# Kernel optimization log

Measured on AMD Instinct MI355X. Metric: run time of the kernel, lower is better.

The kernel has to match this reference:

```python
import jax, jax.numpy as jnp
import numpy as np

# DeepSpeed FixedSparsityConfig defaults (attention='unidirectional')
BLOCK = 16
NUM_LOCAL_BLOCKS = 4   # local window = 4 blocks = 64 tokens
D_MODEL = 1024
N_HEADS = 16
HEAD_DIM = D_MODEL // N_HEADS


def _block_layout(seq_len: int) -> np.ndarray:
    """Token-level boolean mask [S,S] from the fixed unidirectional block layout.
    Allowed iff: (same 4-block local window AND block_k <= block_q) OR
                 (block_k % 4 == 3 AND block_k <= block_q)  (causal global column).
    Same layout for every head (different_layout_per_head=False)."""
    nb = seq_len // BLOCK
    r = np.arange(nb)
    causal = r[None, :] <= r[:, None]
    same_win = (r[:, None] // NUM_LOCAL_BLOCKS) == (r[None, :] // NUM_LOCAL_BLOCKS)
    glob = (r[None, :] % NUM_LOCAL_BLOCKS) == (NUM_LOCAL_BLOCKS - 1)
    layout = (same_win & causal) | (glob & causal)
    return np.kron(layout, np.ones((BLOCK, BLOCK), dtype=bool))


def setup_inputs() -> dict:
    key = jax.random.key(0)
    ks = jax.random.split(key, 7)
    B, S = 2, 2048
    init = 1.0 / np.sqrt(D_MODEL)
    x = jax.random.normal(ks[0], (B, S, D_MODEL), jnp.float32)
    key_padding_mask = jnp.zeros((B, S), jnp.float32)  # additive mask ('add' mode)
    Wq = jax.random.normal(ks[1], (D_MODEL, D_MODEL), jnp.float32) * init
    Wk = jax.random.normal(ks[2], (D_MODEL, D_MODEL), jnp.float32) * init
    Wv = jax.random.normal(ks[3], (D_MODEL, D_MODEL), jnp.float32) * init
    bq = jax.random.normal(ks[4], (D_MODEL,), jnp.float32) * 0.01
    bk = jax.random.normal(ks[5], (D_MODEL,), jnp.float32) * 0.01
    bv = jax.random.normal(ks[6], (D_MODEL,), jnp.float32) * 0.01
    return dict(x=x, key_padding_mask=key_padding_mask,
                Wq=Wq, bq=bq, Wk=Wk, bk=bk, Wv=Wv, bv=bv)


def reference(x, key_padding_mask, Wq, bq, Wk, bk, Wv, bv):
    B, S, D = x.shape
    q = (x @ Wq + bq).reshape(B, S, N_HEADS, HEAD_DIM)
    k = (x @ Wk + bk).reshape(B, S, N_HEADS, HEAD_DIM)
    v = (x @ Wv + bv).reshape(B, S, N_HEADS, HEAD_DIM)
    scale = HEAD_DIM ** -0.5  # DeepSpeed scales by head_size**-0.5 inside softmax
    scores = jnp.einsum('bqhd,bkhd->bhqk', q, k) * scale
    scores = scores + key_padding_mask[:, None, None, :]
    mask = jnp.asarray(_block_layout(S))  # [S,S] bool; absent blocks excluded from softmax
    scores = jnp.where(mask[None, None], scores, -jnp.inf)
    attn = jax.nn.softmax(scores, axis=-1)
    out = jnp.einsum('bhqk,bkhd->bqhd', attn, v)
    return out.reshape(B, S, D)
```

## Files before the change

kernel.cpp:

```cpp
#include <hip/hip_runtime.h>
#include <hip/hip_bf16.h>

typedef __bf16 bf16;
typedef __bf16 bf16x4 __attribute__((ext_vector_type(4)));
typedef __bf16 bf16x8 __attribute__((ext_vector_type(8)));
typedef float  f32x4  __attribute__((ext_vector_type(4)));

#define D_MODEL 1024
#define S_LEN   2048
#define BATCH   2
#define NH      16
#define HD      64
#define NX ((size_t)BATCH * S_LEN * D_MODEL)

__device__ inline void gl_lds16(const bf16* g, bf16* l) {
    __builtin_amdgcn_global_load_lds(
        (const __attribute__((address_space(1))) void*)g,
        (__attribute__((address_space(3))) void*)l, 16, 0, 0);
}

__global__ __launch_bounds__(256) void cvt_x(
    const float* __restrict__ x, bf16* __restrict__ xb)
{
    const size_t base = ((size_t)blockIdx.x * 256 + threadIdx.x) * 8;
    const float4 a = *(const float4*)(x + base);
    const float4 b = *(const float4*)(x + base + 4);
    bf16x8 o;
    o[0] = (bf16)a.x; o[1] = (bf16)a.y; o[2] = (bf16)a.z; o[3] = (bf16)a.w;
    o[4] = (bf16)b.x; o[5] = (bf16)b.y; o[6] = (bf16)b.z; o[7] = (bf16)b.w;
    *(bf16x8*)(xb + base) = o;
}

__global__ __launch_bounds__(256) void wt_cvt(
    const float* __restrict__ Wq, const float* __restrict__ Wk,
    const float* __restrict__ Wv, bf16* __restrict__ Wt)
{
    const int z = blockIdx.z;
    const float* W = (z == 0) ? Wq : (z == 1) ? Wk : Wv;
    const int k0 = blockIdx.y * 64, n0 = blockIdx.x * 64;

    __shared__ bf16 tile[64 * 72];

    const int r16 = threadIdx.x >> 4, c4 = (threadIdx.x & 15) << 2;

#pragma unroll
    for (int rr = 0; rr < 4; ++rr) {
        const int row = rr * 16 + r16;
        const float4 v = *(const float4*)(W + (size_t)(k0 + row) * D_MODEL + n0 + c4);
        bf16x4 o; o[0] = (bf16)v.x; o[1] = (bf16)v.y; o[2] = (bf16)v.z; o[3] = (bf16)v.w;
        *(bf16x4*)(tile + row * 72 + c4) = o;
    }
    __syncthreads();
#pragma unroll
    for (int rr = 0; rr < 4; ++rr) {
        const int row = rr * 16 + r16;
        bf16x4 o;
#pragma unroll
        for (int j = 0; j < 4; ++j) o[j] = tile[(c4 + j) * 72 + row];
        *(bf16x4*)(Wt + (size_t)(z * D_MODEL + n0 + row) * D_MODEL + k0 + c4) = o;
    }
}

__global__ __launch_bounds__(256) void gemm_bt(
    const bf16* __restrict__ Xb, const bf16* __restrict__ Wt,
    const float* __restrict__ bq, const float* __restrict__ bk,
    const float* __restrict__ bv, bf16* __restrict__ QKV)
{
    const int n0 = blockIdx.x * 128, m0 = blockIdx.y * 128;
    const int z  = n0 >> 10;
    const float* bias = (z == 0) ? bq : (z == 1) ? bk : bv;
    const float scale = (z == 0) ? 0.125f : 1.0f;
    bf16* C = QKV + (size_t)z * NX;
    const int ncol0 = n0 & 1023;

    __shared__ bf16 As[128 * 32];
    __shared__ bf16 Bs[128 * 32];

    const int t = threadIdx.x, wave = t >> 6, lane = t & 63;
    const int wm = wave >> 1, wn = wave & 1;
    const int col = lane & 15, quad = lane >> 4;
    const int srow = t >> 2, sc8 = (t & 3) << 3;

    f32x4 acc[4][4] = {};

    for (int k0 = 0; k0 < D_MODEL; k0 += 32) {
        gl_lds16(Xb + (size_t)(m0 + srow) * D_MODEL + k0 + sc8,      As + wave * 512);
        gl_lds16(Xb + (size_t)(m0 + 64 + srow) * D_MODEL + k0 + sc8, As + 2048 + wave * 512);
        gl_lds16(Wt + (size_t)(n0 + srow) * D_MODEL + k0 + sc8,      Bs + wave * 512);
        gl_lds16(Wt + (size_t)(n0 + 64 + srow) * D_MODEL + k0 + sc8, Bs + 2048 + wave * 512);
        __syncthreads();

        bf16x8 a[4], b[4];
#pragma unroll
        for (int mt = 0; mt < 4; ++mt)
            a[mt] = *(const bf16x8*)(As + (wm * 64 + mt * 16 + col) * 32 + quad * 8);
#pragma unroll
        for (int nt = 0; nt < 4; ++nt)
            b[nt] = *(const bf16x8*)(Bs + (wn * 64 + nt * 16 + col) * 32 + quad * 8);
#pragma unroll
        for (int mt = 0; mt < 4; ++mt)
#pragma unroll
            for (int nt = 0; nt < 4; ++nt)
                acc[mt][nt] = __builtin_amdgcn_mfma_f32_16x16x32_bf16(a[mt], b[nt], acc[mt][nt], 0, 0, 0);
        __syncthreads();
    }

#pragma unroll
    for (int nt = 0; nt < 4; ++nt) {
        const int cgw = ncol0 + wn * 64 + nt * 16 + col;
        const float bsv = bias[cgw];
#pragma unroll
        for (int mt = 0; mt < 4; ++mt)
#pragma unroll
            for (int i = 0; i < 4; ++i) {
                const int rg = m0 + wm * 64 + mt * 16 + quad * 4 + i;
                C[(size_t)rg * D_MODEL + cgw] = (bf16)((acc[mt][nt][i] + bsv) * scale);
            }
    }
}

__global__ __launch_bounds__(256) void sparse_attn64(
    const bf16* __restrict__ Q, const bf16* __restrict__ Kv,
    const bf16* __restrict__ Vv, const float* __restrict__ kpm,
    float* __restrict__ out)
{
    const int w = (gridDim.x - 1) - blockIdx.x;
    const int h = blockIdx.y, b = blockIdx.z;
    const int t = threadIdx.x, wavei = t >> 6, lane = t & 63;
    const int col = lane & 15, quad = lane >> 4;
    const int qb = 4 * w + wavei;

    __shared__ bf16 KbS[2][64 * 72];
    __shared__ bf16 VtS[2][64 * 72];
    __shared__ bf16 Ps[4][16 * 72];

    const size_t qrow = ((size_t)(b * S_LEN + qb * 16 + col)) * D_MODEL + h * HD;
    const bf16x8 aq0 = *(const bf16x8*)(Q + qrow + quad * 8);
    const bf16x8 aq1 = *(const bf16x8*)(Q + qrow + 32 + quad * 8);

    f32x4 o[4] = {};
    float lacc[4] = {0.f, 0.f, 0.f, 0.f};

    const int nGlob = (w + 3) >> 2;
    const int niter = nGlob + 1;

    const int srow = t >> 2, sd16 = (t & 3) << 4;
    const int sg = srow >> 4, sr = srow & 15;
    const int p2 = t & 31, dg8 = (t >> 5) << 3;
    const int key0 = 2 * p2, vg = key0 >> 4, vr = key0 & 15;

    auto kb_of = [&](int it, int g) -> int {
        if (it == nGlob) return 4 * w + g;
        const int j = 4 * it + g;
        return (j < w) ? (4 * j + 3) : 3;
    };

    bf16x8 rk0, rk1, rv0, rv1;
    {
        const size_t krow = ((size_t)(b * S_LEN + kb_of(0, sg) * 16 + sr)) * D_MODEL + h * HD + sd16;
        rk0 = *(const bf16x8*)(Kv + krow);
        rk1 = *(const bf16x8*)(Kv + krow + 8);
        const size_t vrow = ((size_t)(b * S_LEN + kb_of(0, vg) * 16 + vr)) * D_MODEL + h * HD + dg8;
        rv0 = *(const bf16x8*)(Vv + vrow);
        rv1 = *(const bf16x8*)(Vv + vrow + D_MODEL);
        *(bf16x8*)(KbS[0] + srow * 72 + sd16)     = rk0;
        *(bf16x8*)(KbS[0] + srow * 72 + sd16 + 8) = rk1;
#pragma unroll
        for (int j = 0; j < 8; ++j) {
            bf16 pr[2] = { rv0[j], rv1[j] };
            *(unsigned int*)(VtS[0] + (dg8 + j) * 72 + key0) = *(unsigned int*)pr;
        }
    }

    for (int it = 0; it < niter; ++it) {
        __syncthreads();
        const int cur = it & 1, nxt = cur ^ 1;
        const bool more = (it + 1 < niter);
        if (more) {
            const size_t krow = ((size_t)(b * S_LEN + kb_of(it + 1, sg) * 16 + sr)) * D_MODEL + h * HD + sd16;
            rk0 = *(const bf16x8*)(Kv + krow);
            rk1 = *(const bf16x8*)(Kv + krow + 8);
            const size_t vrow = ((size_t)(b * S_LEN + kb_of(it + 1, vg) * 16 + vr)) * D_MODEL + h * HD + dg8;
            rv0 = *(const bf16x8*)(Vv + vrow);
            rv1 = *(const bf16x8*)(Vv + vrow + D_MODEL);
        }

        const bf16* Kb = KbS[cur];
        const bf16* Vt = VtS[cur];

        f32x4 s[4];
        float mval[4];
        bool  val[4];
#pragma unroll
        for (int g = 0; g < 4; ++g) {
            int kb;
            if (it == nGlob) { kb = 4 * w + g; val[g] = (g <= wavei); }
            else { const int j = 4 * it + g; val[g] = (j < w); kb = val[g] ? (4 * j + 3) : 3; }
            mval[g] = kpm[b * S_LEN + kb * 16 + col];
            f32x4 z = {};
            const bf16x8 bk0 = *(const bf16x8*)(Kb + (g * 16 + col) * 72 + quad * 8);
            const bf16x8 bk1 = *(const bf16x8*)(Kb + (g * 16 + col) * 72 + 32 + quad * 8);
            z = __builtin_amdgcn_mfma_f32_16x16x32_bf16(aq0, bk0, z, 0, 0, 0);
            s[g] = __builtin_amdgcn_mfma_f32_16x16x32_bf16(aq1, bk1, z, 0, 0, 0);
        }

#pragma unroll
        for (int i = 0; i < 4; ++i) {
#pragma unroll
            for (int g = 0; g < 4; ++g) {
                const float si = val[g] ? (s[g][i] + mval[g]) : -1e30f;
                const float pv = __expf(si);
                lacc[i] += pv;
                Ps[wavei][(quad * 4 + i) * 72 + g * 16 + col] = (bf16)pv;
            }
        }

        const bf16x8 aP0 = *(const bf16x8*)(Ps[wavei] + col * 72 + quad * 8);
        const bf16x8 aP1 = *(const bf16x8*)(Ps[wavei] + col * 72 + 32 + quad * 8);
#pragma unroll
        for (int nt = 0; nt < 4; ++nt) {
            const bf16x8 b0 = *(const bf16x8*)(Vt + (nt * 16 + col) * 72 + quad * 8);
            const bf16x8 b1 = *(const bf16x8*)(Vt + (nt * 16 + col) * 72 + 32 + quad * 8);
            o[nt] = __builtin_amdgcn_mfma_f32_16x16x32_bf16(aP0, b0, o[nt], 0, 0, 0);
            o[nt] = __builtin_amdgcn_mfma_f32_16x16x32_bf16(aP1, b1, o[nt], 0, 0, 0);
        }

        if (more) {
            *(bf16x8*)(KbS[nxt] + srow * 72 + sd16)     = rk0;
            *(bf16x8*)(KbS[nxt] + srow * 72 + sd16 + 8) = rk1;
#pragma unroll
            for (int j = 0; j < 8; ++j) {
                bf16 pr[2] = { rv0[j], rv1[j] };
                *(unsigned int*)(VtS[nxt] + (dg8 + j) * 72 + key0) = *(unsigned int*)pr;
            }
        }
    }

#pragma unroll
    for (int i = 0; i < 4; ++i) {
        float rs = lacc[i];
        rs += __shfl_xor(rs, 1);
        rs += __shfl_xor(rs, 2);
        rs += __shfl_xor(rs, 4);
        rs += __shfl_xor(rs, 8);
        const float inv = 1.0f / rs;
        const int rg = b * S_LEN + qb * 16 + quad * 4 + i;
#pragma unroll
        for (int nt = 0; nt < 4; ++nt)
            out[(size_t)rg * D_MODEL + h * HD + nt * 16 + col] = o[nt][i] * inv;
    }
}

extern "C" void kernel_launch(void* const* d_in, const int* in_sizes, int n_in,
                              void* d_out, int out_size, void* d_ws, size_t ws_size,
                              hipStream_t stream)
{
    const float* x = nullptr; const float* kpm = nullptr;
    const float* Wp[3] = {nullptr, nullptr, nullptr};
    const float* bp[3] = {nullptr, nullptr, nullptr};
    int wn = 0, bn = 0;
    for (int i = 0; i < n_in; ++i) {
        const float* p = (const float*)d_in[i];
        const long s = in_sizes[i];
        if (s == (long)NX)            x = p;
        else if (s == BATCH * S_LEN)  kpm = p;
        else if (s == D_MODEL * D_MODEL && wn < 3) Wp[wn++] = p;
        else if (s == D_MODEL && bn < 3)           bp[bn++] = p;
    }

    bf16* Qb = (bf16*)d_ws;
    bf16* Kb = Qb + NX;
    bf16* Vb = Kb + NX;
    bf16* Xb = (bf16*)d_out;
    bf16* Wt = Xb + NX;
    float* outp = (float*)d_out;

    cvt_x<<<(int)(NX / 8 / 256), 256, 0, stream>>>(x, Xb);
    wt_cvt<<<dim3(16, 16, 3), 256, 0, stream>>>(Wp[0], Wp[1], Wp[2], Wt);

    gemm_bt<<<dim3(3 * D_MODEL / 128, (BATCH * S_LEN) / 128), 256, 0, stream>>>(
        Xb, Wt, bp[0], bp[1], bp[2], Qb);

    sparse_attn64<<<dim3(S_LEN / 64, NH, BATCH), 256, 0, stream>>>(
        Qb, Kb, Vb, kpm, outp);
}
```

Measured before the change: 159.2 us.

## Merge conversion kernels, remap GEMM tiles per XCD, load K directly from global

```diff
diff --git a/kernel.cpp b/kernel.cpp
--- a/kernel.cpp
+++ b/kernel.cpp
@@ -19,28 +19,28 @@
         (__attribute__((address_space(3))) void*)l, 16, 0, 0);
 }
 
-__global__ __launch_bounds__(256) void cvt_x(
-    const float* __restrict__ x, bf16* __restrict__ xb)
-{
-    const size_t base = ((size_t)blockIdx.x * 256 + threadIdx.x) * 8;
-    const float4 a = *(const float4*)(x + base);
-    const float4 b = *(const float4*)(x + base + 4);
-    bf16x8 o;
-    o[0] = (bf16)a.x; o[1] = (bf16)a.y; o[2] = (bf16)a.z; o[3] = (bf16)a.w;
-    o[4] = (bf16)b.x; o[5] = (bf16)b.y; o[6] = (bf16)b.z; o[7] = (bf16)b.w;
-    *(bf16x8*)(xb + base) = o;
-}
-
-__global__ __launch_bounds__(256) void wt_cvt(
+__global__ __launch_bounds__(256) void cvt_all(
+    const float* __restrict__ x,
     const float* __restrict__ Wq, const float* __restrict__ Wk,
-    const float* __restrict__ Wv, bf16* __restrict__ Wt)
-{
-    const int z = blockIdx.z;
+    const float* __restrict__ Wv,
+    bf16* __restrict__ xb, bf16* __restrict__ Wt)
+{
+    if (blockIdx.x < 2048) {
+        const size_t base = ((size_t)blockIdx.x * 256 + threadIdx.x) * 8;
+        const float4 a = *(const float4*)(x + base);
+        const float4 b = *(const float4*)(x + base + 4);
+        bf16x8 o;
+        o[0] = (bf16)a.x; o[1] = (bf16)a.y; o[2] = (bf16)a.z; o[3] = (bf16)a.w;
+        o[4] = (bf16)b.x; o[5] = (bf16)b.y; o[6] = (bf16)b.z; o[7] = (bf16)b.w;
+        *(bf16x8*)(xb + base) = o;
+        return;
+    }
+    const int id = blockIdx.x - 2048;
+    const int z = id / 256, tid = id % 256;
+    const int k0 = (tid >> 4) * 64, n0 = (tid & 15) * 64;
     const float* W = (z == 0) ? Wq : (z == 1) ? Wk : Wv;
-    const int k0 = blockIdx.y * 64, n0 = blockIdx.x * 64;
 
     __shared__ bf16 tile[64 * 72];
-
     const int r16 = threadIdx.x >> 4, c4 = (threadIdx.x & 15) << 2;
 
 #pragma unroll
@@ -66,7 +66,10 @@
     const float* __restrict__ bq, const float* __restrict__ bk,
     const float* __restrict__ bv, bf16* __restrict__ QKV)
 {
-    const int n0 = blockIdx.x * 128, m0 = blockIdx.y * 128;
+    const int id  = blockIdx.y * gridDim.x + blockIdx.x;
+    const int xcd = id & 7, rem = id >> 3;
+    const int ntile = xcd * 3 + (rem % 3), mtile = rem / 3;
+    const int n0 = ntile * 128, m0 = mtile * 128;
     const int z  = n0 >> 10;
     const float* bias = (z == 0) ? bq : (z == 1) ? bk : bv;
     const float scale = (z == 0) ? 0.125f : 1.0f;
@@ -130,7 +133,6 @@
     const int col = lane & 15, quad = lane >> 4;
     const int qb = 4 * w + wavei;
 
-    __shared__ bf16 KbS[2][64 * 72];
     __shared__ bf16 VtS[2][64 * 72];
     __shared__ bf16 Ps[4][16 * 72];
 
@@ -144,8 +146,6 @@
     const int nGlob = (w + 3) >> 2;
     const int niter = nGlob + 1;
 
-    const int srow = t >> 2, sd16 = (t & 3) << 4;
-    const int sg = srow >> 4, sr = srow & 15;
     const int p2 = t & 31, dg8 = (t >> 5) << 3;
     const int key0 = 2 * p2, vg = key0 >> 4, vr = key0 & 15;
 
@@ -155,16 +155,11 @@
         return (j < w) ? (4 * j + 3) : 3;
     };
 
-    bf16x8 rk0, rk1, rv0, rv1;
+    bf16x8 rv0, rv1;
     {
-        const size_t krow = ((size_t)(b * S_LEN + kb_of(0, sg) * 16 + sr)) * D_MODEL + h * HD + sd16;
-        rk0 = *(const bf16x8*)(Kv + krow);
-        rk1 = *(const bf16x8*)(Kv + krow + 8);
         const size_t vrow = ((size_t)(b * S_LEN + kb_of(0, vg) * 16 + vr)) * D_MODEL + h * HD + dg8;
         rv0 = *(const bf16x8*)(Vv + vrow);
         rv1 = *(const bf16x8*)(Vv + vrow + D_MODEL);
-        *(bf16x8*)(KbS[0] + srow * 72 + sd16)     = rk0;
-        *(bf16x8*)(KbS[0] + srow * 72 + sd16 + 8) = rk1;
 #pragma unroll
         for (int j = 0; j < 8; ++j) {
             bf16 pr[2] = { rv0[j], rv1[j] };
@@ -177,15 +172,10 @@
         const int cur = it & 1, nxt = cur ^ 1;
         const bool more = (it + 1 < niter);
         if (more) {
-            const size_t krow = ((size_t)(b * S_LEN + kb_of(it + 1, sg) * 16 + sr)) * D_MODEL + h * HD + sd16;
-            rk0 = *(const bf16x8*)(Kv + krow);
-            rk1 = *(const bf16x8*)(Kv + krow + 8);
             const size_t vrow = ((size_t)(b * S_LEN + kb_of(it + 1, vg) * 16 + vr)) * D_MODEL + h * HD + dg8;
             rv0 = *(const bf16x8*)(Vv + vrow);
             rv1 = *(const bf16x8*)(Vv + vrow + D_MODEL);
         }
-
-        const bf16* Kb = KbS[cur];
         const bf16* Vt = VtS[cur];
 
         f32x4 s[4];
@@ -197,9 +187,10 @@
             if (it == nGlob) { kb = 4 * w + g; val[g] = (g <= wavei); }
             else { const int j = 4 * it + g; val[g] = (j < w); kb = val[g] ? (4 * j + 3) : 3; }
             mval[g] = kpm[b * S_LEN + kb * 16 + col];
+            const bf16* kp = Kv + ((size_t)(b * S_LEN + kb * 16 + col)) * D_MODEL + h * HD;
+            const bf16x8 bk0 = *(const bf16x8*)(kp + quad * 8);
+            const bf16x8 bk1 = *(const bf16x8*)(kp + 32 + quad * 8);
             f32x4 z = {};
-            const bf16x8 bk0 = *(const bf16x8*)(Kb + (g * 16 + col) * 72 + quad * 8);
-            const bf16x8 bk1 = *(const bf16x8*)(Kb + (g * 16 + col) * 72 + 32 + quad * 8);
             z = __builtin_amdgcn_mfma_f32_16x16x32_bf16(aq0, bk0, z, 0, 0, 0);
             s[g] = __builtin_amdgcn_mfma_f32_16x16x32_bf16(aq1, bk1, z, 0, 0, 0);
         }
@@ -226,8 +217,6 @@
         }
 
         if (more) {
-            *(bf16x8*)(KbS[nxt] + srow * 72 + sd16)     = rk0;
-            *(bf16x8*)(KbS[nxt] + srow * 72 + sd16 + 8) = rk1;
 #pragma unroll
             for (int j = 0; j < 8; ++j) {
                 bf16 pr[2] = { rv0[j], rv1[j] };
@@ -275,11 +264,9 @@
     bf16* Wt = Xb + NX;
     float* outp = (float*)d_out;
 
-    cvt_x<<<(int)(NX / 8 / 256), 256, 0, stream>>>(x, Xb);
-    wt_cvt<<<dim3(16, 16, 3), 256, 0, stream>>>(Wp[0], Wp[1], Wp[2], Wt);
-
-    gemm_bt<<<dim3(3 * D_MODEL / 128, (BATCH * S_LEN) / 128), 256, 0, stream>>>(
-        Xb, Wt, bp[0], bp[1], bp[2], Qb);
+    cvt_all<<<2048 + 768, 256, 0, stream>>>(x, Wp[0], Wp[1], Wp[2], Xb, Wt);
+
+    gemm_bt<<<dim3(24, 32), 256, 0, stream>>>(Xb, Wt, bp[0], bp[1], bp[2], Qb);
 
     sparse_attn64<<<dim3(S_LEN / 64, NH, BATCH), 256, 0, stream>>>(
         Qb, Kb, Vb, kpm, outp);
```

New measurement: 171.1 us. +7.5%, slower.
